# Kernel optimization log

Hardware: AMD Instinct MI355X
Metric: run time of the kernel (lower is better)

The kernel has to match this reference:

```python
import jax, jax.numpy as jnp
import numpy as np

DT = 1.0
SPIKE_THRESHOLD = 30.0


def setup_inputs() -> dict:
    key = jax.random.key(0)
    kx, = jax.random.split(key, 1)
    x = jax.random.normal(kx, (16, 64, 1024, 32), dtype=jnp.float32)
    # scalar learnable parameters (Izhikevich model constants)
    a = jnp.float32(0.02)
    b = jnp.float32(0.2)
    c = jnp.float32(-65.0)
    d = jnp.float32(8.0)
    return {"x": x, "a": a, "b": b, "c": c, "d": d}


def reference(x, a, b, c, d):
    # x: [B, C, N, T]. Initial membrane potential v and recovery u are zeros.
    B, C, N, T = x.shape
    v0 = jnp.zeros((B, C, N), dtype=x.dtype)
    u0 = jnp.zeros((B, C, N), dtype=x.dtype)
    xs = jnp.moveaxis(x, -1, 0)  # [T, B, C, N] time-major for scan

    def step(carry, x_t):
        v, u = carry
        dv = 0.04 * v * v + 5.0 * v + 140.0 - u + x_t
        v = v + DT * dv
        du = a * (b * v - u)
        u = u + DT * du
        spike = (v >= SPIKE_THRESHOLD).astype(x_t.dtype)
        v = v * (1.0 - spike) + c * spike
        u = u + d * spike
        return (v, u), spike

    (_, _), spikes = jax.lax.scan(step, (v0, u0), xs)
    return jnp.moveaxis(spikes, 0, -1)  # [B, C, N, T]
```

## Files before the change

kernel.cpp:

```cpp
#include <hip/hip_runtime.h>


#define T_STEPS 32
#define TPB 256
#define ROW 33

__global__ __launch_bounds__(TPB) void izhikevich_kernel(
    const float* __restrict__ x,
    const float* __restrict__ pa,
    const float* __restrict__ pb,
    const float* __restrict__ pc,
    const float* __restrict__ pd,
    float* __restrict__ out)
{
#pragma clang fp contract(off)
    __shared__ float lds[TPB * ROW];

    const int t = threadIdx.x;
    const size_t blockBase = (size_t)blockIdx.x * (TPB * T_STEPS);

    const float a = pa[0];
    const float b = pb[0];
    const float c = pc[0];
    const float d = pd[0];

    const float4* __restrict__ xin =
        reinterpret_cast<const float4*>(x + blockBase);
#pragma unroll
    for (int k = 0; k < 8; ++k) {
        const float4 ch = xin[k * TPB + t];
        const int ng = k * 32 + (t >> 3);
        const int tg = (t & 7) * 4;
        float* row = &lds[ng * ROW + tg];
        row[0] = ch.x; row[1] = ch.y; row[2] = ch.z; row[3] = ch.w;
    }
    __syncthreads();

    float xs[T_STEPS];
#pragma unroll
    for (int j = 0; j < T_STEPS; ++j) xs[j] = lds[t * ROW + j];

    float v = 0.0f;
    float u = 0.0f;
#pragma unroll
    for (int j = 0; j < T_STEPS; ++j) {
        const float xt = xs[j];
        const float t1 = (0.04f * v) * v;
        const float t2 = 5.0f * v;
        const float dv = (((t1 + t2) + 140.0f) - u) + xt;
        v = v + dv;
        const float du = a * ((b * v) - u);
        u = u + du;
        const float spike = (v >= 30.0f) ? 1.0f : 0.0f;
        const float oms = 1.0f - spike;
        v = (v * oms) + (c * spike);
        u = u + (d * spike);
        lds[t * ROW + j] = spike;
    }
    __syncthreads();

    float4* __restrict__ op = reinterpret_cast<float4*>(out + blockBase);
#pragma unroll
    for (int k = 0; k < 8; ++k) {
        const int ng = k * 32 + (t >> 3);
        const int tg = (t & 7) * 4;
        const float* row = &lds[ng * ROW + tg];
        float4 o;
        o.x = row[0]; o.y = row[1]; o.z = row[2]; o.w = row[3];
        op[k * TPB + t] = o;
    }
}

extern "C" void kernel_launch(void* const* d_in, const int* in_sizes, int n_in,
                              void* d_out, int out_size, void* d_ws, size_t ws_size,
                              hipStream_t stream) {
    const float* x  = (const float*)d_in[0];
    const float* pa = (const float*)d_in[1];
    const float* pb = (const float*)d_in[2];
    const float* pc = (const float*)d_in[3];
    const float* pd = (const float*)d_in[4];
    float* out = (float*)d_out;

    const int n_neurons = in_sizes[0] / T_STEPS;
    const int grid = n_neurons / TPB;

    izhikevich_kernel<<<grid, TPB, 0, stream>>>(x, pa, pb, pc, pd, out);
}
```

Before: 239.5 us.

## Shrink blocks to one wavefront and vectorize LDS transpose with float4 accesses

```diff
diff --git a/kernel.cpp b/kernel.cpp
--- a/kernel.cpp
+++ b/kernel.cpp
@@ -2,8 +2,8 @@
 
 
 #define T_STEPS 32
-#define TPB 256
-#define ROW 33
+#define TPB 64
+#define ROW 36
 
 __global__ __launch_bounds__(TPB) void izhikevich_kernel(
     const float* __restrict__ x,
@@ -17,56 +17,63 @@
     __shared__ float lds[TPB * ROW];
 
     const int t = threadIdx.x;
-    const size_t blockBase = (size_t)blockIdx.x * (TPB * T_STEPS);
+    const size_t base = (size_t)blockIdx.x * (TPB * T_STEPS);
 
     const float a = pa[0];
     const float b = pb[0];
     const float c = pc[0];
     const float d = pd[0];
 
-    const float4* __restrict__ xin =
-        reinterpret_cast<const float4*>(x + blockBase);
+    const float4* __restrict__ xin = reinterpret_cast<const float4*>(x + base);
+    float4 ch[8];
+#pragma unroll
+    for (int k = 0; k < 8; ++k) ch[k] = xin[k * TPB + t];
+
 #pragma unroll
     for (int k = 0; k < 8; ++k) {
-        const float4 ch = xin[k * TPB + t];
-        const int ng = k * 32 + (t >> 3);
+        const int ng = k * 8 + (t >> 3);
         const int tg = (t & 7) * 4;
-        float* row = &lds[ng * ROW + tg];
-        row[0] = ch.x; row[1] = ch.y; row[2] = ch.z; row[3] = ch.w;
+        *reinterpret_cast<float4*>(&lds[ng * ROW + tg]) = ch[k];
     }
     __syncthreads();
 
     float xs[T_STEPS];
 #pragma unroll
-    for (int j = 0; j < T_STEPS; ++j) xs[j] = lds[t * ROW + j];
+    for (int j = 0; j < 8; ++j)
+        *reinterpret_cast<float4*>(&xs[j * 4]) =
+            *reinterpret_cast<const float4*>(&lds[t * ROW + j * 4]);
 
     float v = 0.0f;
     float u = 0.0f;
 #pragma unroll
-    for (int j = 0; j < T_STEPS; ++j) {
-        const float xt = xs[j];
-        const float t1 = (0.04f * v) * v;
-        const float t2 = 5.0f * v;
-        const float dv = (((t1 + t2) + 140.0f) - u) + xt;
-        v = v + dv;
-        const float du = a * ((b * v) - u);
-        u = u + du;
-        const float spike = (v >= 30.0f) ? 1.0f : 0.0f;
-        const float oms = 1.0f - spike;
-        v = (v * oms) + (c * spike);
-        u = u + (d * spike);
-        lds[t * ROW + j] = spike;
+    for (int j = 0; j < 8; ++j) {
+        float4 sp;
+        float* sf = reinterpret_cast<float*>(&sp);
+#pragma unroll
+        for (int i = 0; i < 4; ++i) {
+            const float xt = xs[j * 4 + i];
+            const float t1 = (0.04f * v) * v;
+            const float t2 = 5.0f * v;
+            const float dv = (((t1 + t2) + 140.0f) - u) + xt;
+            v = v + dv;
+            const float du = a * ((b * v) - u);
+            u = u + du;
+            const float spike = (v >= 30.0f) ? 1.0f : 0.0f;
+            const float oms = 1.0f - spike;
+            v = (v * oms) + (c * spike);
+            u = u + (d * spike);
+            sf[i] = spike;
+        }
+        *reinterpret_cast<float4*>(&lds[t * ROW + j * 4]) = sp;
     }
     __syncthreads();
 
-    float4* __restrict__ op = reinterpret_cast<float4*>(out + blockBase);
+    float4* __restrict__ op = reinterpret_cast<float4*>(out + base);
 #pragma unroll
     for (int k = 0; k < 8; ++k) {
-        const int ng = k * 32 + (t >> 3);
+        const int ng = k * 8 + (t >> 3);
         const int tg = (t & 7) * 4;
-        const float* row = &lds[ng * ROW + tg];
-        float4 o;
-        o.x = row[0]; o.y = row[1]; o.z = row[2]; o.w = row[3];
+        const float4 o = *reinterpret_cast<const float4*>(&lds[ng * ROW + tg]);
         op[k * TPB + t] = o;
     }
 }
```

Result: no change. 238.9 us (-0.2%).
